# Kernel optimization log

Hardware: AMD Instinct MI355X
Metric: run time of the kernel (lower is better)

The kernel has to match this reference:

```python
import jax, jax.numpy as jnp
import numpy as np

B, N, K = 8, 2048, 20
EPS = 1e-8
BN_EPS = 1e-5

def knn(x, k):
    # x: (B,N,C); top-k by negative squared euclidean distance (DGCNN knn)
    xx = jnp.sum(x * x, axis=-1)
    inner = jnp.einsum('bnc,bmc->bnm', x, x)
    neg_d = 2.0 * inner - xx[:, :, None] - xx[:, None, :]
    _, idx = jax.lax.top_k(neg_d, k)
    return idx  # (B,N,k)

def gather_neighbors(x, idx):
    b = jnp.arange(x.shape[0])[:, None, None]
    return x[b, idx]  # (B,N,k,C)

def rot_to_z(n):
    # Rodrigues rotation taking unit normal n -> z=(0,0,1); n: (B,N,3)
    vx, vy = n[..., 1], -n[..., 0]  # v = n x z = (ny, -nx, 0)
    c = n[..., 2]
    z = jnp.zeros_like(c)
    Km = jnp.stack([z, z, vy, z, z, -vx, -vy, vx, z], axis=-1).reshape(n.shape[:-1] + (3, 3))
    I = jnp.eye(3, dtype=n.dtype)
    s = 1.0 / jnp.maximum(1.0 + c, EPS)
    return I + Km + jnp.einsum('bnij,bnjk->bnik', Km, Km) * s[..., None, None]

def bn_lrelu(h, g, b):
    # training-mode BatchNorm2d (biased var over B,N,K) + LeakyReLU(0.2); h: (B,C,N,K)
    m = jnp.mean(h, axis=(0, 2, 3), keepdims=True)
    v = jnp.mean((h - m) ** 2, axis=(0, 2, 3), keepdims=True)
    y = (h - m) * jax.lax.rsqrt(v + BN_EPS) * g[None, :, None, None] + b[None, :, None, None]
    return jnp.where(y > 0, y, 0.2 * y)

def graph_feature_3d(x, normals, idx):
    feat = gather_neighbors(x, idx)                # (B,N,K,3)
    diff = feat - x[:, :, None, :]                 # neighbor offsets
    R1 = rot_to_z(normals)                         # (B,N,3,3)
    rot = jnp.einsum('bnij,bnkj->bnki', R1, diff)  # rotate offsets into normal-aligned frame
    # Rotation_fix_axis_mirror: rotate about fixed z-axis so the neighborhood mean
    # aligns with +x, and append the xz-plane mirrored copy (2*num_dims features).
    mvec = jnp.mean(rot, axis=2)                   # (B,N,3)
    theta = jnp.arctan2(mvec[..., 1], mvec[..., 0])
    ct, st = jnp.cos(theta), jnp.sin(theta)
    z = jnp.zeros_like(ct); o = jnp.ones_like(ct)
    R2 = jnp.stack([ct, st, z, -st, ct, z, z, z, o], axis=-1).reshape(ct.shape + (3, 3))
    rot2 = jnp.einsum('bnij,bnkj->bnki', R2, rot)
    mir = rot2 * jnp.array([1.0, -1.0, 1.0], rot2.dtype)
    x_rep = jnp.broadcast_to(x[:, :, None, :], feat.shape)
    f = jnp.concatenate([rot2, mir, x_rep], axis=-1)   # (B,N,K,9)
    return jnp.transpose(f, (0, 3, 1, 2)), R1, R2      # (B,9,N,K)

def graph_feature(x, idx):
    feat = gather_neighbors(x, idx)
    x_rep = jnp.broadcast_to(x[:, :, None, :], feat.shape)
    f = jnp.concatenate([feat - x_rep, x_rep], axis=-1)  # (B,N,K,2C)
    return jnp.transpose(f, (0, 3, 1, 2))

def setup_inputs():
    key = jax.random.key(0)
    ks = jax.random.split(key, 5)
    x = jax.random.normal(ks[0], (B, N, 3), jnp.float32)
    nrm = jax.random.normal(ks[1], (B, N, 3), jnp.float32)
    normals = nrm / jnp.linalg.norm(nrm, axis=-1, keepdims=True)
    def w(k, o, c):
        return jax.random.normal(k, (o, c), jnp.float32) * np.float32(np.sqrt(2.0 / c))
    return {
        'x': x, 'normals': normals,
        'conv1_w': w(ks[2], 64, 9),
        'bn1_g': jnp.ones((64,), jnp.float32), 'bn1_b': jnp.zeros((64,), jnp.float32),
        'conv2_w': w(ks[3], 128, 128),
        'bn2_g': jnp.ones((128,), jnp.float32), 'bn2_b': jnp.zeros((128,), jnp.float32),
        'conv3_w': w(ks[4], 256, 256),
        'bn3_g': jnp.ones((256,), jnp.float32), 'bn3_b': jnp.zeros((256,), jnp.float32),
    }

def reference(x, normals, conv1_w, bn1_g, bn1_b, conv2_w, bn2_g, bn2_b, conv3_w, bn3_g, bn3_b):
    idx = knn(x, K)
    f, R1, R2 = graph_feature_3d(x, normals, idx)
    h = bn_lrelu(jnp.einsum('oc,bcnk->bonk', conv1_w, f), bn1_g, bn1_b)
    x1 = jnp.transpose(jnp.max(h, axis=-1), (0, 2, 1))   # (B,N,64)
    f = graph_feature(x1, idx)                            # reuse coordinate kNN
    h = bn_lrelu(jnp.einsum('oc,bcnk->bonk', conv2_w, f), bn2_g, bn2_b)
    x2 = jnp.transpose(jnp.max(h, axis=-1), (0, 2, 1))   # (B,N,128)
    f = graph_feature(x2, knn(x2, K))                     # fresh kNN in feature space
    h = bn_lrelu(jnp.einsum('oc,bcnk->bonk', conv3_w, f), bn3_g, bn3_b)
    x3 = jnp.transpose(jnp.max(h, axis=-1), (0, 2, 1))   # (B,N,256)
    return jnp.concatenate([x1, x2, x3], axis=-1), R1, R2
```

## Files before the change

### kernel.cpp

```cpp
#include <hip/hip_runtime.h>
#include <hip/hip_bf16.h>
#include <math.h>

namespace {

constexpr int B  = 8;
constexpr int N  = 2048;
constexpr int K  = 20;
constexpr int C1 = 64, C2 = 128, C3 = 256;
constexpr int NSLICE = 64;
constexpr double COUNT = 327680.0;
constexpr double BNEPS = 1e-5;

constexpr size_t OFF_IDX1  = 0;
constexpr size_t OFF_IDX2  = OFF_IDX1 + (size_t)B*N*K*4;
constexpr size_t OFF_X1D   = OFF_IDX2 + (size_t)B*N*K*4;
constexpr size_t OFF_X2D   = OFF_X1D  + (size_t)B*N*C1*8;
constexpr size_t OFF_STATS = OFF_X2D  + (size_t)B*N*C2*8;
constexpr size_t OFF_MI    = OFF_STATS+ (size_t)2*NSLICE*C3*8;
constexpr size_t OFF_X2F   = OFF_MI   + 4096;
constexpr size_t OFF_XX2F  = OFF_X2F  + (size_t)B*N*C2*4;
constexpr size_t OFF_WPK   = OFF_XX2F + (size_t)B*N*4;
constexpr size_t OFF_BIG   = OFF_WPK  + 65536;

typedef short  bf16x8 __attribute__((ext_vector_type(8)));
typedef float  f32x4  __attribute__((ext_vector_type(4)));

__device__ __forceinline__ float fmul32(float a, float b){ return __fmul_rn(a,b); }
__device__ __forceinline__ float fadd32(float a, float b){ return __fadd_rn(a,b); }
__device__ __forceinline__ float fsub32(float a, float b){ return __fsub_rn(a,b); }

__global__ __launch_bounds__(256) void knn_xyz_wave(const float* __restrict__ x,
                                                    int* __restrict__ idxo) {
  int row  = blockIdx.x * 4 + (threadIdx.x >> 6);
  int lane = threadIdx.x & 63;
  int b = row >> 11, n = row & (N - 1);
  const float* xb = x + (size_t)b * N * 3;
  float xi0 = xb[(size_t)n*3], xi1 = xb[(size_t)n*3+1], xi2 = xb[(size_t)n*3+2];
  float xxi = fadd32(fadd32(fmul32(xi0,xi0), fmul32(xi1,xi1)), fmul32(xi2,xi2));
  float vals[32];
  #pragma unroll
  for (int t = 0; t < 32; ++t) {
    int j = lane + (t << 6);
    float a = xb[(size_t)j*3], c = xb[(size_t)j*3+1], d = xb[(size_t)j*3+2];
    float xxj   = fadd32(fadd32(fmul32(a,a), fmul32(c,c)), fmul32(d,d));
    float inner = fadd32(fadd32(fmul32(xi0,a), fmul32(xi1,c)), fmul32(xi2,d));
    vals[t] = fsub32(fsub32(fmul32(2.f, inner), xxi), xxj);
  }
  int* out = idxo + (size_t)row * K;
  for (int sel = 0; sel < K; ++sel) {
    float best = -INFINITY; int bt = 0;
    #pragma unroll
    for (int t = 0; t < 32; ++t)
      if (vals[t] > best) { best = vals[t]; bt = t; }
    int bcol = lane + (bt << 6);
    #pragma unroll
    for (int off = 32; off >= 1; off >>= 1) {
      float ov = __shfl_xor(best, off, 64);
      int   oc = __shfl_xor(bcol, off, 64);
      if (ov > best || (ov == best && oc < bcol)) { best = ov; bcol = oc; }
    }
    if (lane == 0) out[sel] = bcol;
    int kill = ((bcol & 63) == lane) ? (bcol >> 6) : 32;
    #pragma unroll
    for (int t = 0; t < 32; ++t) if (t == kill) vals[t] = -INFINITY;
  }
}

__global__ __launch_bounds__(64) void xx2f_kernel(const double* __restrict__ x2d,
                                                  float* __restrict__ x2f,
                                                  float* __restrict__ xx2f) {
  int row = blockIdx.x * 64 + threadIdx.x;
  const double* src = x2d + (size_t)row * C2;
  float* dst = x2f + (size_t)row * C2;
  float sq[C2];
  #pragma unroll 8
  for (int c = 0; c < C2; ++c) {
    float v = (float)src[c];
    dst[c] = v;
    sq[c] = fmul32(v, v);
  }
  float r0=sq[0], r1=sq[1], r2=sq[2], r3=sq[3], r4=sq[4], r5=sq[5], r6=sq[6], r7=sq[7];
  #pragma unroll
  for (int i = 8; i < 128; i += 8) {
    r0 = fadd32(r0, sq[i+0]); r1 = fadd32(r1, sq[i+1]);
    r2 = fadd32(r2, sq[i+2]); r3 = fadd32(r3, sq[i+3]);
    r4 = fadd32(r4, sq[i+4]); r5 = fadd32(r5, sq[i+5]);
    r6 = fadd32(r6, sq[i+6]); r7 = fadd32(r7, sq[i+7]);
  }
  xx2f[row] = fadd32(fadd32(fadd32(r0,r1), fadd32(r2,r3)),
                     fadd32(fadd32(r4,r5), fadd32(r6,r7)));
}

__global__ __launch_bounds__(256) void dist_f32_kernel(const float* __restrict__ x2f,
                                                       const float* __restrict__ xx2f,
                                                       float* __restrict__ dist) {
  int bz = blockIdx.z;
  const float* x2b  = x2f  + (size_t)bz * N * C2;
  const float* xx2b = xx2f + (size_t)bz * N;
  float* db = dist + (size_t)bz * N * N;
  int ti = blockIdx.y * 64;
  int tj = blockIdx.x * 64;
  int tid = threadIdx.x;
  int tr = tid >> 4, tc = tid & 15;
  __shared__ float A[64][9], Bm[64][9];
  float acc[4][4];
  #pragma unroll
  for (int u = 0; u < 4; ++u)
    #pragma unroll
    for (int v = 0; v < 4; ++v) acc[u][v] = 0.f;
  for (int c0 = 0; c0 < C2; c0 += 8) {
    for (int i = tid; i < 512; i += 256) {
      int r = i >> 3, c = i & 7;
      A[r][c]  = x2b[(size_t)(ti + r)*C2 + c0 + c];
      Bm[r][c] = x2b[(size_t)(tj + r)*C2 + c0 + c];
    }
    __syncthreads();
    #pragma unroll
    for (int c = 0; c < 8; ++c) {
      float a[4], bv[4];
      #pragma unroll
      for (int u = 0; u < 4; ++u) a[u] = A[tr*4 + u][c];
      #pragma unroll
      for (int v = 0; v < 4; ++v) bv[v] = Bm[tc*4 + v][c];
      #pragma unroll
      for (int u = 0; u < 4; ++u)
        #pragma unroll
        for (int v = 0; v < 4; ++v)
          acc[u][v] = fadd32(acc[u][v], fmul32(a[u], bv[v]));
    }
    __syncthreads();
  }
  #pragma unroll
  for (int u = 0; u < 4; ++u) {
    int i = ti + tr*4 + u;
    float xxi = xx2b[i];
    #pragma unroll
    for (int v = 0; v < 4; ++v) {
      int j = tj + tc*4 + v;
      db[(size_t)i*N + j] = fsub32(fsub32(fmul32(2.f, acc[u][v]), xxi), xx2b[j]);
    }
  }
}

__global__ __launch_bounds__(256) void knn_feat_wave(const float* __restrict__ dist,
                                                     int* __restrict__ idxo) {
  int row  = blockIdx.x * 4 + (threadIdx.x >> 6);
  int lane = threadIdx.x & 63;
  const float* dr = dist + (size_t)row * N;
  float vals[32];
  #pragma unroll
  for (int t = 0; t < 32; ++t) vals[t] = dr[lane + (t << 6)];
  int* out = idxo + (size_t)row * K;
  for (int sel = 0; sel < K; ++sel) {
    float best = -INFINITY; int bt = 0;
    #pragma unroll
    for (int t = 0; t < 32; ++t)
      if (vals[t] > best) { best = vals[t]; bt = t; }
    int bcol = lane + (bt << 6);
    #pragma unroll
    for (int off = 32; off >= 1; off >>= 1) {
      float ov = __shfl_xor(best, off, 64);
      int   oc = __shfl_xor(bcol, off, 64);
      if (ov > best || (ov == best && oc < bcol)) { best = ov; bcol = oc; }
    }
    if (lane == 0) out[sel] = bcol;
    int kill = ((bcol & 63) == lane) ? (bcol >> 6) : 32;
    #pragma unroll
    for (int t = 0; t < 32; ++t) if (t == kill) vals[t] = -INFINITY;
  }
}

__global__ __launch_bounds__(64) void l1_p0(
    const float* __restrict__ x, const float* __restrict__ nrm,
    const float* __restrict__ w1, const int* __restrict__ idx1,
    double* __restrict__ sS, double* __restrict__ sQ,
    double* __restrict__ hmx1, double* __restrict__ hmn1,
    float* __restrict__ outR1, float* __restrict__ outR2) {
  int p = blockIdx.x;
  int tid = threadIdx.x;
  int b = p >> 11, n = p & (N - 1);
  __shared__ float  wl[C1 * 9];
  __shared__ double rotd[K][3];
  __shared__ double fld[K][9];
  for (int i = tid; i < C1 * 9; i += 64) wl[i] = w1[i];
  const float* xb = x + (size_t)b * N * 3;
  double nx = nrm[(size_t)p*3], ny = nrm[(size_t)p*3+1], nz = nrm[(size_t)p*3+2];
  double vx = ny, vy = -nx;
  double s = 1.0 / fmax(1.0 + nz, 1e-8);
  double vxy = vx * vy;
  double R1v[9];
  R1v[0] = 1.0 - s*(vy*vy); R1v[1] = s*vxy;           R1v[2] = vy;
  R1v[3] = s*vxy;           R1v[4] = 1.0 - s*(vx*vx); R1v[5] = -vx;
  R1v[6] = -vy;             R1v[7] = vx;              R1v[8] = 1.0 - s*(vx*vx + vy*vy);
  double xi0 = xb[(size_t)n*3], xi1 = xb[(size_t)n*3+1], xi2 = xb[(size_t)n*3+2];
  if (tid < K) {
    int j = idx1[(size_t)p*K + tid];
    double d0 = (double)xb[(size_t)j*3]   - xi0;
    double d1 = (double)xb[(size_t)j*3+1] - xi1;
    double d2 = (double)xb[(size_t)j*3+2] - xi2;
    rotd[tid][0] = R1v[0]*d0 + R1v[1]*d1 + R1v[2]*d2;
    rotd[tid][1] = R1v[3]*d0 + R1v[4]*d1 + R1v[5]*d2;
    rotd[tid][2] = R1v[6]*d0 + R1v[7]*d1 + R1v[8]*d2;
  }
  __syncthreads();
  double mx = 0.0, my = 0.0;
  #pragma unroll
  for (int k = 0; k < K; ++k) { mx += rotd[k][0]; my += rotd[k][1]; }
  mx /= 20.0; my /= 20.0;
  double r = sqrt(mx*mx + my*my);
  double ct = 1.0, st = 0.0;
  if (r > 0.0) { ct = mx / r; st = my / r; }
  if (tid < K) {
    double r0 = rotd[tid][0], r1 = rotd[tid][1], r2 = rotd[tid][2];
    double a0 = ct*r0 + st*r1;
    double a1 = ct*r1 - st*r0;
    fld[tid][0] = a0;  fld[tid][1] = a1;   fld[tid][2] = r2;
    fld[tid][3] = a0;  fld[tid][4] = -a1;  fld[tid][5] = r2;
    fld[tid][6] = xi0; fld[tid][7] = xi1;  fld[tid][8] = xi2;
  }
  if (tid == 0) {
    float* o1 = outR1 + (size_t)p * 9;
    #pragma unroll
    for (int i = 0; i < 9; ++i) o1[i] = (float)R1v[i];
    float* o2 = outR2 + (size_t)p * 9;
    o2[0] = (float)ct;  o2[1] = (float)st; o2[2] = 0.f;
    o2[3] = (float)-st; o2[4] = (float)ct; o2[5] = 0.f;
    o2[6] = 0.f;        o2[7] = 0.f;       o2[8] = 1.f;
  }
  __syncthreads();
  int o = tid;
  double sum = 0., sq = 0., hmx = -INFINITY, hmn = INFINITY;
  #pragma unroll
  for (int k = 0; k < K; ++k) {
    double h = 0.;
    #pragma unroll
    for (int c = 0; c < 9; ++c) h = fma((double)wl[o*9 + c], fld[k][c], h);
    sum += h; sq += h*h;
    hmx = fmax(hmx, h); hmn = fmin(hmn, h);
  }
  hmx1[(size_t)p*C1 + o] = hmx;
  hmn1[(size_t)p*C1 + o] = hmn;
  int slice = p & (NSLICE - 1);
  atomicAdd(&sS[slice*C3 + o], sum);
  atomicAdd(&sQ[slice*C3 + o], sq);
}

__global__ __launch_bounds__(256) void l1_p1_light(
    const double* __restrict__ hmx1, const double* __restrict__ hmn1,
    const double* __restrict__ mid, const float* __restrict__ g1,
    const float* __restrict__ b1,
    double* __restrict__ x1d, float* __restrict__ out448) {
  int i = blockIdx.x * 256 + threadIdx.x;
  int p = i >> 6, o = i & 63;
  double m = mid[o], is = mid[C3 + o];
  double g = g1[o], bb = b1[o];
  double y1 = ((hmx1[i] - m) * is) * g + bb;
  y1 = y1 > 0.0 ? y1 : 0.2 * y1;
  double y2 = ((hmn1[i] - m) * is) * g + bb;
  y2 = y2 > 0.0 ? y2 : 0.2 * y2;
  double mxv = fmax(y1, y2);
  x1d[i] = mxv;
  out448[(size_t)p*448 + o] = (float)mxv;
}

__device__ __forceinline__ void conv2_core(const double* __restrict__ x1d,
                                           const int* __restrict__ idx,
                                           const float* __restrict__ w,
                                           int p, int tid, double (&acc)[K]) {
  int b = p >> 11;
  __shared__ double difL[K][C1];
  __shared__ double xiL[C1];
  __shared__ int jidx[K];
  if (tid < K) jidx[tid] = idx[(size_t)p*K + tid];
  if (tid < C1) xiL[tid] = x1d[(size_t)p*C1 + tid];
  __syncthreads();
  #pragma unroll 1
  for (int i = tid; i < K*C1; i += 128) {
    int k = i >> 6, c = i & 63;
    difL[k][c] = x1d[((size_t)b*N + jidx[k])*C1 + c] - xiL[c];
  }
  __syncthreads();
  const float* wr = w + (size_t)tid * (2*C1);
  #pragma unroll
  for (int k = 0; k < K; ++k) acc[k] = 0.0;
  #pragma unroll
  for (int c0 = 0; c0 < C1; c0 += 16) {
    double wd[16];
    #pragma unroll
    for (int i = 0; i < 16; ++i) wd[i] = (double)wr[c0+i];
    #pragma unroll
    for (int k = 0; k < K; ++k) {
      #pragma unroll
      for (int i = 0; i < 16; ++i) acc[k] = fma(wd[i], difL[k][c0+i], acc[k]);
    }
  }
  #pragma unroll
  for (int c0 = 0; c0 < C1; c0 += 16) {
    double wd[16], xiv[16];
    #pragma unroll
    for (int i = 0; i < 16; ++i) { wd[i] = (double)wr[C1+c0+i]; xiv[i] = xiL[c0+i]; }
    #pragma unroll
    for (int k = 0; k < K; ++k) {
      #pragma unroll
      for (int i = 0; i < 16; ++i) acc[k] = fma(wd[i], xiv[i], acc[k]);
    }
  }
}

__global__ __launch_bounds__(128, 1) void conv2_p0(
    const double* __restrict__ x1d, const int* __restrict__ idx,
    const float* __restrict__ w,
    double* __restrict__ sS, double* __restrict__ sQ,
    double* __restrict__ hmx2, double* __restrict__ hmn2) {
  int p = blockIdx.x;
  int tid = threadIdx.x;
  double acc[K];
  conv2_core(x1d, idx, w, p, tid, acc);
  double sum = 0., sq = 0., hmx = -INFINITY, hmn = INFINITY;
  #pragma unroll
  for (int k = 0; k < K; ++k) {
    sum += acc[k]; sq += acc[k]*acc[k];
    hmx = fmax(hmx, acc[k]); hmn = fmin(hmn, acc[k]);
  }
  hmx2[(size_t)p*C2 + tid] = hmx;
  hmn2[(size_t)p*C2 + tid] = hmn;
  int slice = p & (NSLICE - 1);
  atomicAdd(&sS[slice*C3 + tid], sum);
  atomicAdd(&sQ[slice*C3 + tid], sq);
}

__global__ __launch_bounds__(256) void conv2_p1_light(
    const double* __restrict__ hmx2, const double* __restrict__ hmn2,
    const double* __restrict__ mid, const float* __restrict__ gam,
    const float* __restrict__ bet,
    double* __restrict__ x2d, float* __restrict__ out448) {
  int i = blockIdx.x * 256 + threadIdx.x;
  int p = i >> 7, o = i & 127;
  double m = mid[o], is = mid[C3 + o];
  double g = gam[o], bb = bet[o];
  double y1 = ((hmx2[i] - m) * is) * g + bb;
  y1 = y1 > 0.0 ? y1 : 0.2 * y1;
  double y2 = ((hmn2[i] - m) * is) * g + bb;
  y2 = y2 > 0.0 ? y2 : 0.2 * y2;
  double mxv = fmax(y1, y2);
  x2d[i] = mxv;
  out448[(size_t)p*448 + C1 + o] = (float)mxv;
}

__global__ __launch_bounds__(256) void wpack_kernel(const float* __restrict__ w,
                                                    bf16x8* __restrict__ wpk) {
  int idx = blockIdx.x * 256 + threadIdx.x;
  int lane = idx & 63;
  int ks = (idx >> 6) & 3;
  int nt = idx >> 8;
  int oc = nt*16 + (lane & 15);
  int g = lane >> 4;
  const float* src = w + (size_t)oc * (2*C2) + ks*32 + g*8;
  bf16x8 pk;
  #pragma unroll
  for (int e = 0; e < 8; ++e) {
    __hip_bfloat16 hb = __float2bfloat16(src[e]);
    pk[e] = *reinterpret_cast<short*>(&hb);
  }
  wpk[idx] = pk;
}

__global__ __launch_bounds__(256) void base_kernel(const float* __restrict__ x2f,
                                                   const float* __restrict__ w,
                                                   float* __restrict__ baseB) {
  int to = blockIdx.x * 64;
  int tp = blockIdx.y * 64;
  int tid = threadIdx.x;
  int tr = tid >> 4, tc = tid & 15;
  __shared__ float A[64][9], Bm[64][9];
  float acc[4][4];
  #pragma unroll
  for (int u = 0; u < 4; ++u)
    #pragma unroll
    for (int v = 0; v < 4; ++v) acc[u][v] = 0.f;
  for (int c0 = 0; c0 < C2; c0 += 8) {
    for (int i = tid; i < 512; i += 256) {
      int r = i >> 3, c = i & 7;
      A[r][c]  = x2f[(size_t)(tp + r)*C2 + c0 + c];
      const float* wr = w + (size_t)(to + r) * (2*C2);
      Bm[r][c] = wr[C2 + c0 + c] - wr[c0 + c];
    }
    __syncthreads();
    #pragma unroll
    for (int c = 0; c < 8; ++c) {
      float a[4], bv[4];
      #pragma unroll
      for (int u = 0; u < 4; ++u) a[u] = A[tr*4 + u][c];
      #pragma unroll
      for (int v = 0; v < 4; ++v) bv[v] = Bm[tc*4 + v][c];
      #pragma unroll
      for (int u = 0; u < 4; ++u)
        #pragma unroll
        for (int v = 0; v < 4; ++v) acc[u][v] = fmaf(a[u], bv[v], acc[u][v]);
    }
    __syncthreads();
  }
  #pragma unroll
  for (int u = 0; u < 4; ++u) {
    #pragma unroll
    for (int v = 0; v < 4; ++v)
      baseB[(size_t)(tp + tr*4 + u)*C3 + to + tc*4 + v] = acc[u][v];
  }
}

__global__ __launch_bounds__(256, 1) void conv3_p0_mfma(
    const float* __restrict__ x2f, const int* __restrict__ idx,
    const bf16x8* __restrict__ wpk, const float* __restrict__ baseB,
    double* __restrict__ sS, double* __restrict__ sQ,
    float* __restrict__ hmx3, float* __restrict__ hmn3) {
  int p = blockIdx.x;
  int tid = threadIdx.x;
  int lane = tid & 63;
  int wv = tid >> 6;
  int b = p >> 11;
  __shared__ float4 xjB4[32 * 16];
  __shared__ int    jidx[K];
  if (tid < K) jidx[tid] = idx[(size_t)p*K + tid];
  __syncthreads();
  #pragma unroll 1
  for (int i = tid; i < 320; i += 256) {
    int row = i >> 4, slot = i & 15;
    const float* src = x2f + ((size_t)b*N + jidx[row])*C2 + slot*8;
    bf16x8 pk;
    #pragma unroll
    for (int e = 0; e < 8; ++e) {
      __hip_bfloat16 hb = __float2bfloat16(src[e]);
      pk[e] = *reinterpret_cast<short*>(&hb);
    }
    *reinterpret_cast<bf16x8*>(&xjB4[row*16 + (slot ^ (row & 15))]) = pk;
  }
  __syncthreads();
  bf16x8 afrag[2][4];
  #pragma unroll
  for (int mt = 0; mt < 2; ++mt) {
    #pragma unroll
    for (int ks = 0; ks < 4; ++ks) {
      int row = mt*16 + (lane & 15);
      int slot = ks*4 + (lane >> 4);
      afrag[mt][ks] = *reinterpret_cast<const bf16x8*>(&xjB4[row*16 + (slot ^ (row & 15))]);
    }
  }
  int slice = p & (NSLICE - 1);
  int g = lane >> 4;
  #pragma unroll 1
  for (int nt = wv; nt < 16; nt += 4) {
    int oc = nt*16 + (lane & 15);
    f32x4 acc0 = {0.f, 0.f, 0.f, 0.f};
    f32x4 acc1 = {0.f, 0.f, 0.f, 0.f};
    #pragma unroll
    for (int ks = 0; ks < 4; ++ks) {
      bf16x8 bw = wpk[nt*256 + ks*64 + lane];
      acc0 = __builtin_amdgcn_mfma_f32_16x16x32_bf16(afrag[0][ks], bw, acc0, 0, 0, 0);
      acc1 = __builtin_amdgcn_mfma_f32_16x16x32_bf16(afrag[1][ks], bw, acc1, 0, 0, 0);
    }
    float bs = baseB[(size_t)p*C3 + oc];
    float s = 0.f, q = 0.f, mxv = -INFINITY, mnv = INFINITY;
    #pragma unroll
    for (int r = 0; r < 4; ++r) {
      float h = bs + acc0[r];
      s += h; q += h*h;
      mxv = fmaxf(mxv, h); mnv = fminf(mnv, h);
    }
    if (g == 0) {
      #pragma unroll
      for (int r = 0; r < 4; ++r) {
        float h = bs + acc1[r];
        s += h; q += h*h;
        mxv = fmaxf(mxv, h); mnv = fminf(mnv, h);
      }
    }
    #pragma unroll
    for (int off = 16; off <= 32; off <<= 1) {
      s += __shfl_xor(s, off, 64);
      q += __shfl_xor(q, off, 64);
      mxv = fmaxf(mxv, __shfl_xor(mxv, off, 64));
      mnv = fminf(mnv, __shfl_xor(mnv, off, 64));
    }
    if (g == 0) {
      hmx3[(size_t)p*C3 + oc] = mxv;
      hmn3[(size_t)p*C3 + oc] = mnv;
      atomicAdd(&sS[slice*C3 + oc], (double)s);
      atomicAdd(&sQ[slice*C3 + oc], (double)q);
    }
  }
}

__global__ __launch_bounds__(256) void conv3_p1_light(
    const float* __restrict__ hmx3, const float* __restrict__ hmn3,
    const double* __restrict__ mid, const float* __restrict__ gam,
    const float* __restrict__ bet, float* __restrict__ out448) {
  int i = blockIdx.x * 256 + threadIdx.x;
  int p = i >> 8, o = i & 255;
  float m = (float)mid[o], is = (float)mid[C3 + o];
  float g = gam[o], bb = bet[o];
  float y1 = (hmx3[i] - m) * is * g + bb;
  y1 = y1 > 0.f ? y1 : 0.2f * y1;
  float y2 = (hmn3[i] - m) * is * g + bb;
  y2 = y2 > 0.f ? y2 : 0.2f * y2;
  out448[(size_t)p*448 + C1 + C2 + o] = fmaxf(y1, y2);
}

__global__ void finalize_stats(const double* __restrict__ sS, const double* __restrict__ sQ,
                               double* __restrict__ mid, int C) {
  int o = threadIdx.x;
  if (o >= C) return;
  double s = 0., q = 0.;
  for (int i = 0; i < NSLICE; ++i) { s += sS[i*C3 + o]; q += sQ[i*C3 + o]; }
  double m = s / COUNT;
  double v = q / COUNT - m*m;
  mid[o] = m;
  mid[C3 + o] = 1.0 / sqrt(v + BNEPS);
}

}

extern "C" void kernel_launch(void* const* d_in, const int* in_sizes, int n_in,
                              void* d_out, int out_size, void* d_ws, size_t ws_size,
                              hipStream_t stream) {
  (void)in_sizes; (void)n_in; (void)out_size; (void)ws_size;
  const float* x   = (const float*)d_in[0];
  const float* nrm = (const float*)d_in[1];
  const float* w1  = (const float*)d_in[2];
  const float* g1  = (const float*)d_in[3];
  const float* b1  = (const float*)d_in[4];
  const float* w2  = (const float*)d_in[5];
  const float* g2  = (const float*)d_in[6];
  const float* b2  = (const float*)d_in[7];
  const float* w3  = (const float*)d_in[8];
  const float* g3  = (const float*)d_in[9];
  const float* b3  = (const float*)d_in[10];
  float* out = (float*)d_out;
  char*  ws  = (char*)d_ws;

  int*    idx1 = (int*)(ws + OFF_IDX1);
  int*    idx2 = (int*)(ws + OFF_IDX2);
  double* x1d  = (double*)(ws + OFF_X1D);
  double* x2d  = (double*)(ws + OFF_X2D);
  double* sS   = (double*)(ws + OFF_STATS);
  double* sQ   = sS + (size_t)NSLICE * C3;
  double* mid  = (double*)(ws + OFF_MI);
  float*  x2f  = (float*)(ws + OFF_X2F);
  float*  xx2f = (float*)(ws + OFF_XX2F);
  bf16x8* wpk  = (bf16x8*)(ws + OFF_WPK);
  char*   big  = ws + OFF_BIG;
  double* hmx1 = (double*)big;
  double* hmn1 = hmx1 + (size_t)B*N*C1;
  double* hmx2 = (double*)big;
  double* hmn2 = hmx2 + (size_t)B*N*C2;
  float*  dist = (float*)big;
  float*  hmx3 = (float*)big;
  float*  hmn3 = hmx3 + (size_t)B*N*C3;
  float*  baseB = hmn3 + (size_t)B*N*C3;

  float* outR1 = out + (size_t)B * N * 448;
  float* outR2 = outR1 + (size_t)B * N * 9;

  wpack_kernel<<<16, 256, 0, stream>>>(w3, wpk);

  knn_xyz_wave<<<B*N/4, 256, 0, stream>>>(x, idx1);

  hipMemsetAsync(sS, 0, (size_t)2*NSLICE*C3*sizeof(double), stream);
  l1_p0<<<B*N, 64, 0, stream>>>(x, nrm, w1, idx1, sS, sQ, hmx1, hmn1, outR1, outR2);
  finalize_stats<<<1, C3, 0, stream>>>(sS, sQ, mid, C1);
  l1_p1_light<<<B*N*C1/256, 256, 0, stream>>>(hmx1, hmn1, mid, g1, b1, x1d, out);

  hipMemsetAsync(sS, 0, (size_t)2*NSLICE*C3*sizeof(double), stream);
  conv2_p0<<<B*N, 128, 0, stream>>>(x1d, idx1, w2, sS, sQ, hmx2, hmn2);
  finalize_stats<<<1, C3, 0, stream>>>(sS, sQ, mid, C2);
  conv2_p1_light<<<B*N*C2/256, 256, 0, stream>>>(hmx2, hmn2, mid, g2, b2, x2d, out);

  xx2f_kernel<<<B*N/64, 64, 0, stream>>>(x2d, x2f, xx2f);
  dist_f32_kernel<<<dim3(N/64, N/64, B), 256, 0, stream>>>(x2f, xx2f, dist);
  knn_feat_wave<<<B*N/4, 256, 0, stream>>>(dist, idx2);

  base_kernel<<<dim3(C3/64, B*N/64), 256, 0, stream>>>(x2f, w3, baseB);
  hipMemsetAsync(sS, 0, (size_t)2*NSLICE*C3*sizeof(double), stream);
  conv3_p0_mfma<<<B*N, 256, 0, stream>>>(x2f, idx2, wpk, baseB, sS, sQ, hmx3, hmn3);
  finalize_stats<<<1, C3, 0, stream>>>(sS, sQ, mid, C3);
  conv3_p1_light<<<B*N*C3/256, 256, 0, stream>>>(hmx3, hmn3, mid, g3, b3, out);
}
```

Before: 841.7 us.

## Precompute per-point conv2 base term with (W2b-W1a)·xi in a separate GEMM kernel

Rewrites conv2 as W_a·x_j + (W_b − W_a)·x_i, so the per-neighbor loop only multiplies gathered neighbor features, and the per-point term is computed once by a new tiled double-precision GEMM kernel. This removes the subtraction of x_i per neighbor and the second K-times-replicated FMA loop over the center feature. It adds an extra kernel launch and a B·N·C2 double buffer write/read, and changes the summation order slightly.

Measured after the change: 791.3 us. 1.06x faster.

```diff
diff --git a/kernel.cpp b/kernel.cpp
--- a/kernel.cpp
+++ b/kernel.cpp
@@ -264,24 +264,69 @@
   out448[(size_t)p*448 + o] = (float)mxv;
 }
 
-__device__ __forceinline__ void conv2_core(const double* __restrict__ x1d,
-                                           const int* __restrict__ idx,
-                                           const float* __restrict__ w,
-                                           int p, int tid, double (&acc)[K]) {
+__global__ __launch_bounds__(256) void base2_kernel(const double* __restrict__ x1d,
+                                                    const float* __restrict__ w,
+                                                    double* __restrict__ base2B) {
+  int to = blockIdx.x * 64;
+  int tp = blockIdx.y * 64;
+  int tid = threadIdx.x;
+  int tr = tid >> 4, tc = tid & 15;
+  __shared__ double A[64][9], Bm[64][9];
+  double acc[4][4];
+  #pragma unroll
+  for (int u = 0; u < 4; ++u)
+    #pragma unroll
+    for (int v = 0; v < 4; ++v) acc[u][v] = 0.;
+  for (int c0 = 0; c0 < C1; c0 += 8) {
+    for (int i = tid; i < 512; i += 256) {
+      int r = i >> 3, c = i & 7;
+      A[r][c]  = x1d[(size_t)(tp + r)*C1 + c0 + c];
+      const float* wr = w + (size_t)(to + r) * (2*C1);
+      Bm[r][c] = (double)wr[C1 + c0 + c] - (double)wr[c0 + c];
+    }
+    __syncthreads();
+    #pragma unroll
+    for (int c = 0; c < 8; ++c) {
+      double a[4], bv[4];
+      #pragma unroll
+      for (int u = 0; u < 4; ++u) a[u] = A[tr*4 + u][c];
+      #pragma unroll
+      for (int v = 0; v < 4; ++v) bv[v] = Bm[tc*4 + v][c];
+      #pragma unroll
+      for (int u = 0; u < 4; ++u)
+        #pragma unroll
+        for (int v = 0; v < 4; ++v) acc[u][v] = fma(a[u], bv[v], acc[u][v]);
+    }
+    __syncthreads();
+  }
+  #pragma unroll
+  for (int u = 0; u < 4; ++u) {
+    #pragma unroll
+    for (int v = 0; v < 4; ++v)
+      base2B[(size_t)(tp + tr*4 + u)*C2 + to + tc*4 + v] = acc[u][v];
+  }
+}
+
+__global__ __launch_bounds__(128, 1) void conv2_p0(
+    const double* __restrict__ x1d, const int* __restrict__ idx,
+    const float* __restrict__ w, const double* __restrict__ base2B,
+    double* __restrict__ sS, double* __restrict__ sQ,
+    double* __restrict__ hmx2, double* __restrict__ hmn2) {
+  int p = blockIdx.x;
+  int tid = threadIdx.x;
   int b = p >> 11;
-  __shared__ double difL[K][C1];
-  __shared__ double xiL[C1];
+  __shared__ double xjL[K][C1];
   __shared__ int jidx[K];
   if (tid < K) jidx[tid] = idx[(size_t)p*K + tid];
-  if (tid < C1) xiL[tid] = x1d[(size_t)p*C1 + tid];
   __syncthreads();
   #pragma unroll 1
   for (int i = tid; i < K*C1; i += 128) {
     int k = i >> 6, c = i & 63;
-    difL[k][c] = x1d[((size_t)b*N + jidx[k])*C1 + c] - xiL[c];
+    xjL[k][c] = x1d[((size_t)b*N + jidx[k])*C1 + c];
   }
   __syncthreads();
   const float* wr = w + (size_t)tid * (2*C1);
+  double acc[K];
   #pragma unroll
   for (int k = 0; k < K; ++k) acc[k] = 0.0;
   #pragma unroll
@@ -292,36 +337,16 @@
     #pragma unroll
     for (int k = 0; k < K; ++k) {
       #pragma unroll
-      for (int i = 0; i < 16; ++i) acc[k] = fma(wd[i], difL[k][c0+i], acc[k]);
-    }
-  }
-  #pragma unroll
-  for (int c0 = 0; c0 < C1; c0 += 16) {
-    double wd[16], xiv[16];
-    #pragma unroll
-    for (int i = 0; i < 16; ++i) { wd[i] = (double)wr[C1+c0+i]; xiv[i] = xiL[c0+i]; }
-    #pragma unroll
-    for (int k = 0; k < K; ++k) {
-      #pragma unroll
-      for (int i = 0; i < 16; ++i) acc[k] = fma(wd[i], xiv[i], acc[k]);
-    }
-  }
-}
-
-__global__ __launch_bounds__(128, 1) void conv2_p0(
-    const double* __restrict__ x1d, const int* __restrict__ idx,
-    const float* __restrict__ w,
-    double* __restrict__ sS, double* __restrict__ sQ,
-    double* __restrict__ hmx2, double* __restrict__ hmn2) {
-  int p = blockIdx.x;
-  int tid = threadIdx.x;
-  double acc[K];
-  conv2_core(x1d, idx, w, p, tid, acc);
+      for (int i = 0; i < 16; ++i) acc[k] = fma(wd[i], xjL[k][c0+i], acc[k]);
+    }
+  }
+  double base = base2B[(size_t)p*C2 + tid];
   double sum = 0., sq = 0., hmx = -INFINITY, hmn = INFINITY;
   #pragma unroll
   for (int k = 0; k < K; ++k) {
-    sum += acc[k]; sq += acc[k]*acc[k];
-    hmx = fmax(hmx, acc[k]); hmn = fmin(hmn, acc[k]);
+    double h = acc[k] + base;
+    sum += h; sq += h*h;
+    hmx = fmax(hmx, h); hmn = fmin(hmn, h);
   }
   hmx2[(size_t)p*C2 + tid] = hmx;
   hmn2[(size_t)p*C2 + tid] = hmn;
@@ -553,6 +578,7 @@
   double* hmn1 = hmx1 + (size_t)B*N*C1;
   double* hmx2 = (double*)big;
   double* hmn2 = hmx2 + (size_t)B*N*C2;
+  double* base2B = hmn2 + (size_t)B*N*C2;
   float*  dist = (float*)big;
   float*  hmx3 = (float*)big;
   float*  hmn3 = hmx3 + (size_t)B*N*C3;
@@ -570,8 +596,9 @@
   finalize_stats<<<1, C3, 0, stream>>>(sS, sQ, mid, C1);
   l1_p1_light<<<B*N*C1/256, 256, 0, stream>>>(hmx1, hmn1, mid, g1, b1, x1d, out);
 
+  base2_kernel<<<dim3(C2/64, B*N/64), 256, 0, stream>>>(x1d, w2, base2B);
   hipMemsetAsync(sS, 0, (size_t)2*NSLICE*C3*sizeof(double), stream);
-  conv2_p0<<<B*N, 128, 0, stream>>>(x1d, idx1, w2, sS, sQ, hmx2, hmn2);
+  conv2_p0<<<B*N, 128, 0, stream>>>(x1d, idx1, w2, base2B, sS, sQ, hmx2, hmn2);
   finalize_stats<<<1, C3, 0, stream>>>(sS, sQ, mid, C2);
   conv2_p1_light<<<B*N*C2/256, 256, 0, stream>>>(hmx2, hmn2, mid, g2, b2, x2d, out);
 
```
